# Kernel optimization log

Measured on AMD Instinct MI355X. Metric: run time of the kernel, lower is better.

Reference implementation:

```python
import jax, jax.numpy as jnp
import numpy as np

B, S, IN, OUT, H, M = 16, 512, 512, 512, 8, 4
HF = OUT // H  # head_feats = 64


def setup_inputs() -> dict:
    key = jax.random.key(0)
    ks = jax.random.split(key, 12)
    std = 0.02
    queries = jax.random.normal(ks[0], (B, S, IN), jnp.float32)
    keys = jax.random.normal(ks[1], (B, S, IN), jnp.float32)
    timespans = jax.random.uniform(ks[2], (B, S), jnp.float32)
    # causal mask tiled over heads*batch, matching [H*B, S, S] score shape
    attention_masks = jnp.broadcast_to(jnp.tril(jnp.ones((S, S), jnp.float32)), (H * B, S, S))
    event_marks = jax.random.uniform(ks[3], (H * B, 1, S, M), jnp.float32)
    Wq = std * jax.random.normal(ks[4], (IN, OUT), jnp.float32)
    Wk = std * jax.random.normal(ks[5], (IN, OUT), jnp.float32)
    Wv = std * jax.random.normal(ks[6], (IN, OUT), jnp.float32)
    Wt = std * jax.random.normal(ks[7], (IN, OUT), jnp.float32)
    Wi = std * jax.random.normal(ks[8], (HF + 1, M * HF), jnp.float32)  # fc_i weight
    bi = jnp.zeros((M * HF,), jnp.float32)                               # fc_i bias
    weight_i = std * jax.random.normal(ks[9], (M, HF), jnp.float32)
    scale_i = jnp.zeros((M,), jnp.float32)
    return {"queries": queries, "keys": keys, "timespans": timespans,
            "attention_masks": attention_masks, "event_marks": event_marks,
            "Wq": Wq, "Wk": Wk, "Wv": Wv, "Wt": Wt, "Wi": Wi, "bi": bi,
            "weight_i": weight_i, "scale_i": scale_i}


def reference(queries, keys, timespans, attention_masks, event_marks,
              Wq, Wk, Wv, Wt, Wi, bi, weight_i, scale_i):
    # torch's cat(chunk(X, H, dim=2), dim=0) == [B,S,H,HF] -> [H,B,S,HF] -> flat h*B+b
    def split_heads(X):
        return X.reshape(B, S, H, HF).transpose(2, 0, 1, 3)  # [H,B,S,HF]

    Q = split_heads(queries @ Wq)
    K = split_heads(keys @ Wk)
    V = split_heads(keys @ Wv)
    T = split_heads(keys @ Wt)

    scores = jnp.einsum('hbqf,hbkf->hbqk', Q, K) / jnp.sqrt(jnp.float32(OUT))
    mask = attention_masks.reshape(H, B, S, S)
    scores = jnp.where(mask == 0.0, jnp.float32(-2 ** 32 + 1), scores)
    attn = jax.nn.softmax(scores, axis=-1)  # [H,B,Sq,Sk]

    E = jnp.einsum('hbqk,hbkf->hbqf', attn, T)  # events fed to intensity net

    # --- Hawkes intensities ---
    ts = jnp.broadcast_to(timespans[None, :, :, None], (H, B, S, 1))
    mu = jax.nn.sigmoid(jnp.concatenate([E, ts], axis=-1) @ Wi + bi)  # [H,B,S,M*HF]
    mu = mu.reshape(H, B, S, M, HF)  # chunk over marks along feature dim
    scale = jnp.exp(scale_i)  # [M]
    lam = jnp.einsum('hbsmf,mf->hbsm', mu, weight_i) / scale
    lam = scale * jnp.log1p(jnp.exp(lam))  # scaled softplus, [H,B,S,M]

    # mark_inty[h,b,q,k] = sum_m lam[h,b,q,m] * event_marks[h,b,k,m]
    em = event_marks.reshape(H, B, S, M)
    mark_inty = jnp.einsum('hbqm,hbkm->hbqk', lam, em)

    out = jnp.einsum('hbqk,hbkf->hbqf', attn * mark_inty, V)
    out = out.transpose(1, 2, 0, 3).reshape(B, S, OUT) + queries[..., :OUT]
    all_mark_inty = lam.reshape(H * B, S, M)
    return out, all_mark_inty
```

## Files before the change

### kernel.cpp

```cpp
#include <hip/hip_runtime.h>
#include <math.h>

typedef __attribute__((ext_vector_type(8))) short short8;
typedef __attribute__((ext_vector_type(4))) float f32x4;

static __device__ __forceinline__ unsigned short f2bf(float f) {
  unsigned int u = __float_as_uint(f);
  u += 0x7FFFu + ((u >> 16) & 1u);
  return (unsigned short)(u >> 16);
}

static __device__ __forceinline__ void cp16(void* lds, const void* g) {
  __builtin_amdgcn_global_load_lds((const __attribute__((address_space(1))) void*)g,
                                   (__attribute__((address_space(3))) void*)lds,
                                   16, 0, 0);
}

__global__ __launch_bounds__(256) void convert_k(
    const float* __restrict__ Wq, const float* __restrict__ Wk,
    const float* __restrict__ Wv, const float* __restrict__ Wt,
    const float* __restrict__ Wi,
    unsigned short* __restrict__ Wb, unsigned short* __restrict__ WiF)
{
  __shared__ unsigned short tr[64 * 68];
  const int blk = blockIdx.x, tid = threadIdx.x;
  if (blk < 256) {
    int which = blk >> 6, tile = blk & 63;
    int r0 = (tile >> 3) << 6, c0 = (tile & 7) << 6;
    const float* W = (which == 0) ? Wq : (which == 1) ? Wk : (which == 2) ? Wv : Wt;
    const int rr = tid >> 4, cc = (tid & 15) << 2;
#pragma unroll
    for (int u = 0; u < 4; ++u) {
      int r = rr + u * 16;
      float4 v = *(const float4*)(W + (size_t)(r0 + r) * 512 + c0 + cc);
      tr[(cc + 0) * 68 + r] = f2bf(v.x);
      tr[(cc + 1) * 68 + r] = f2bf(v.y);
      tr[(cc + 2) * 68 + r] = f2bf(v.z);
      tr[(cc + 3) * 68 + r] = f2bf(v.w);
    }
    __syncthreads();
    unsigned short* dst = Wb + which * 262144;
#pragma unroll
    for (int u = 0; u < 4; ++u) {
      int c = rr + u * 16;
      ushort4 o = *(const ushort4*)&tr[c * 68 + cc];
      *(ushort4*)(dst + (size_t)(c0 + c) * 512 + r0 + cc) = o;
    }
  } else {
    int e = (blk - 256) * 256 + tid;
    int j = e & 7, ll = (e >> 3) & 63, r = e >> 9;
    int kk = r % 3, nt = r / 3;
    int col = nt * 16 + (ll & 15);
    int k = kk * 32 + (ll >> 4) * 8 + j;
    float val = (k < 64) ? Wi[k * 256 + col] : ((k == 64) ? Wi[16384 + col] : 0.0f);
    WiF[e] = f2bf(val);
  }
}

__global__ __launch_bounds__(256) void proj_mfma(
    const float* __restrict__ qin, const float* __restrict__ kin,
    const unsigned short* __restrict__ Wb,
    unsigned short* __restrict__ Qg, unsigned short* __restrict__ Kg,
    unsigned short* __restrict__ Vt, unsigned short* __restrict__ Tt)
{
  const int which = blockIdx.z;
  const float* A = (which == 0) ? qin : kin;
  const unsigned short* W = Wb + which * 262144;
  const int row0 = blockIdx.x * 128;
  const int col0 = blockIdx.y * 128;
  const int tid = threadIdx.x;
  const int wv = tid >> 6, l = tid & 63;
  const int quad = l >> 4, lc = l & 15;
  const int wm = wv >> 1, wn = wv & 1;

  __shared__ unsigned short Asm[2][128 * 32];
  __shared__ unsigned short Bsm[2][128 * 32];

  const int e2 = tid + 256;
  const int br0 = tid >> 2, bg0 = (tid & 3) ^ (br0 & 3);
  const int br1 = e2 >> 2,  bg1 = (e2 & 3) ^ (br1 & 3);
  f32x4 acc[4][4] = {};

  cp16(&Bsm[0][tid * 8], W + (size_t)(col0 + br0) * 512 + bg0 * 8);
  cp16(&Bsm[0][e2 * 8], W + (size_t)(col0 + br1) * 512 + bg1 * 8);
#pragma unroll
  for (int u = 0; u < 4; ++u) {
    int i = tid + u * 256, r = i >> 3, c4 = i & 7;
    float4 v = *(const float4*)(A + (size_t)(row0 + r) * 512 + c4 * 4);
    ushort4 o;
    o.x = f2bf(v.x); o.y = f2bf(v.y); o.z = f2bf(v.z); o.w = f2bf(v.w);
    *(ushort4*)&Asm[0][r * 32 + (((c4 >> 1) ^ (r & 3)) << 3) + ((c4 & 1) << 2)] = o;
  }
  __syncthreads();

  const int xk = lc & 3;
  for (int ks = 0; ks < 16; ++ks) {
    const int cur = ks & 1, nxt = cur ^ 1;
    float4 av[4];
    if (ks < 15) {
      const int k1 = (ks + 1) << 5;
      cp16(&Bsm[nxt][tid * 8], W + (size_t)(col0 + br0) * 512 + k1 + bg0 * 8);
      cp16(&Bsm[nxt][e2 * 8], W + (size_t)(col0 + br1) * 512 + k1 + bg1 * 8);
#pragma unroll
      for (int u = 0; u < 4; ++u) {
        int i = tid + u * 256, r = i >> 3, c4 = i & 7;
        av[u] = *(const float4*)(A + (size_t)(row0 + r) * 512 + k1 + c4 * 4);
      }
    }
    short8 a[4], b[4];
#pragma unroll
    for (int mi = 0; mi < 4; ++mi)
      a[mi] = *(const short8*)&Asm[cur][(wm * 64 + mi * 16 + lc) * 32 + ((quad ^ xk) << 3)];
#pragma unroll
    for (int nj = 0; nj < 4; ++nj)
      b[nj] = *(const short8*)&Bsm[cur][(wn * 64 + nj * 16 + lc) * 32 + ((quad ^ xk) << 3)];
#pragma unroll
    for (int mi = 0; mi < 4; ++mi)
#pragma unroll
      for (int nj = 0; nj < 4; ++nj)
        acc[mi][nj] = __builtin_amdgcn_mfma_f32_16x16x32_bf16(a[mi], b[nj], acc[mi][nj], 0, 0, 0);
    if (ks < 15) {
#pragma unroll
      for (int u = 0; u < 4; ++u) {
        int i = tid + u * 256, r = i >> 3, c4 = i & 7;
        ushort4 o;
        o.x = f2bf(av[u].x); o.y = f2bf(av[u].y); o.z = f2bf(av[u].z); o.w = f2bf(av[u].w);
        *(ushort4*)&Asm[nxt][r * 32 + (((c4 >> 1) ^ (r & 3)) << 3) + ((c4 & 1) << 2)] = o;
      }
    }
    __syncthreads();
  }

  const int h = (col0 >> 6) + wn;
  const int bidx = row0 >> 9;
  const int hb = h * 16 + bidx;
  if (which < 2) {
    unsigned short* C = (which == 0) ? Qg : Kg;
    const float os = (which == 0) ? 0.044194173824159216f : 1.0f;
#pragma unroll
    for (int mi = 0; mi < 4; ++mi) {
      int sbase = (row0 & 511) + wm * 64 + mi * 16 + quad * 4;
#pragma unroll
      for (int nj = 0; nj < 4; ++nj) {
        size_t base = (size_t)hb * 32768 + (size_t)sbase * 64 + nj * 16 + lc;
#pragma unroll
        for (int reg = 0; reg < 4; ++reg)
          C[base + (size_t)reg * 64] = f2bf(acc[mi][nj][reg] * os);
      }
    }
  } else {
    unsigned short* C = (which == 2) ? Vt : Tt;
    unsigned short* scr = wn ? Bsm[0] : Asm[0];
    const int sb = (row0 & 511) + wm * 64;
    __syncthreads();
#pragma unroll
    for (int round = 0; round < 2; ++round) {
      if (wm == round) {
#pragma unroll
        for (int mi = 0; mi < 4; ++mi)
#pragma unroll
          for (int nj = 0; nj < 4; ++nj)
#pragma unroll
            for (int reg = 0; reg < 4; ++reg) {
              int f = nj * 16 + lc, s = mi * 16 + quad * 4 + reg;
              int g = (s >> 3) ^ (f & 7);
              scr[f * 64 + g * 8 + (s & 7)] = f2bf(acc[mi][nj][reg]);
            }
#pragma unroll
        for (int it = 0; it < 8; ++it) {
          int fl = it * 8 + (l >> 3);
          int gg = (l & 7) ^ (fl & 7);
          short8 v = *(const short8*)&scr[fl * 64 + gg * 8];
          *(short8*)(C + (size_t)hb * 32768 + (size_t)fl * 512 + sb + (l & 7) * 8) = v;
        }
      }
      __syncthreads();
    }
  }
}

__global__ __launch_bounds__(256, 2) void attn_fused(
    const unsigned short* __restrict__ Qg, const unsigned short* __restrict__ Kg,
    const unsigned short* __restrict__ Vtg, const unsigned short* __restrict__ Ttg,
    const unsigned short* __restrict__ WiF,
    const float* __restrict__ bi, const float* __restrict__ wim,
    const float* __restrict__ sci, const float* __restrict__ tsp,
    const float* __restrict__ em, const float* __restrict__ queries,
    float* __restrict__ out, float* __restrict__ lamout)
{
  const int hb = blockIdx.x;
  const int y = blockIdx.y;
  const int qb = (y == 0) ? 3 : (y == 1) ? 2 : (y == 2) ? 0 : 1;
  const int q0 = qb << 7;
  const int kts = 2 * qb + 2;
  const int tid = threadIdx.x, wv = tid >> 6, l = tid & 63;
  const int quad = l >> 4, lc = l & 15;
  const int xg = lc & 7;

  __shared__ unsigned short Qs[8192];
  __shared__ unsigned short Ks[2][4096];
  __shared__ unsigned short TVs[2][4096];
  __shared__ unsigned short Wl[4][3072];
  __shared__ float emS[2][256];

  const int e1 = tid + 256;
  const int sr0 = tid >> 3, sg0 = (tid & 7) ^ (sr0 & 7);
  const int sr1 = e1 >> 3,  sg1 = (e1 & 7) ^ (sr1 & 7);
  const int sqk0 = sr0 * 64 + sg0 * 8,  sqk1 = sr1 * 64 + sg1 * 8;
  const int stv0 = sr0 * 512 + sg0 * 8, stv1 = sr1 * 512 + sg1 * 8;

  const unsigned short* KgB = Kg + (size_t)hb * 32768;
  const unsigned short* TgB = Ttg + (size_t)hb * 32768;
  const unsigned short* VgB = Vtg + (size_t)hb * 32768;

  const unsigned short* Qbase = Qg + (size_t)hb * 32768 + q0 * 64;
#pragma unroll
  for (int u = 0; u < 4; ++u) {
    int e = tid + u * 256;
    int r = e >> 3, g = (e & 7) ^ (r & 7);
    cp16(&Qs[e * 8], Qbase + r * 64 + g * 8);
  }
  cp16(&Ks[0][tid * 8], KgB + sqk0);
  cp16(&Ks[0][e1 * 8], KgB + sqk1);
  cp16(&TVs[0][tid * 8], TgB + stv0);
  cp16(&TVs[0][e1 * 8], TgB + stv1);
  __syncthreads();

  short8 aq[2][2];
#pragma unroll
  for (int rt = 0; rt < 2; ++rt)
#pragma unroll
    for (int kk = 0; kk < 2; ++kk)
      aq[rt][kk] = *(const short8*)&Qs[(wv * 32 + rt * 16 + lc) * 64 + ((kk * 4 + quad) ^ xg) * 8];

  f32x4 Eacc[2][4] = {};
  float lsum[2][4] = {};
  unsigned int Pc[8][16];

#pragma unroll
  for (int kt = 0; kt < 8; ++kt) {
    if (kt >= kts) continue;
    const int cur = kt & 1, nxt = cur ^ 1;
    const int k0 = kt << 6;
    if (kt + 1 < kts) {
      const int k1 = (kt + 1) << 6;
      cp16(&Ks[nxt][tid * 8], KgB + k1 * 64 + sqk0);
      cp16(&Ks[nxt][e1 * 8], KgB + k1 * 64 + sqk1);
      cp16(&TVs[nxt][tid * 8], TgB + k1 + stv0);
      cp16(&TVs[nxt][e1 * 8], TgB + k1 + stv1);
    }
    f32x4 sc[2][4] = {};
#pragma unroll
    for (int kk = 0; kk < 2; ++kk)
#pragma unroll
      for (int nj = 0; nj < 4; ++nj) {
        short8 b = *(const short8*)&Ks[cur][(nj * 16 + lc) * 64 + ((kk * 4 + quad) ^ xg) * 8];
        sc[0][nj] = __builtin_amdgcn_mfma_f32_16x16x32_bf16(aq[0][kk], b, sc[0][nj], 0, 0, 0);
        sc[1][nj] = __builtin_amdgcn_mfma_f32_16x16x32_bf16(aq[1][kk], b, sc[1][nj], 0, 0, 0);
      }
#pragma unroll
    for (int rt = 0; rt < 2; ++rt) {
      const int gq = q0 + wv * 32 + rt * 16 + quad * 4;
#pragma unroll
      for (int nj = 0; nj < 4; ++nj) {
        int col = nj * 16 + lc;
        unsigned short pb[4];
#pragma unroll
        for (int reg = 0; reg < 4; ++reg) {
          float pv = __expf(sc[rt][nj][reg]);
          if (k0 + col > gq + reg) pv = 0.0f;
          lsum[rt][reg] += pv;
          pb[reg] = f2bf(pv);
          int row = rt * 16 + quad * 4 + reg;
          int gp = (nj * 2 + (lc >> 3)) ^ (row & 7);
          Wl[wv][row * 96 + gp * 8 + (lc & 7)] = pb[reg];
        }
        Pc[kt][(rt * 4 + nj) * 2 + 0] = (unsigned int)pb[0] | ((unsigned int)pb[1] << 16);
        Pc[kt][(rt * 4 + nj) * 2 + 1] = (unsigned int)pb[2] | ((unsigned int)pb[3] << 16);
      }
    }
#pragma unroll
    for (int rt = 0; rt < 2; ++rt)
#pragma unroll
      for (int kk = 0; kk < 2; ++kk) {
        short8 a = *(const short8*)&Wl[wv][(rt * 16 + lc) * 96 + ((kk * 4 + quad) ^ xg) * 8];
#pragma unroll
        for (int fj = 0; fj < 4; ++fj) {
          short8 b = *(const short8*)&TVs[cur][(fj * 16 + lc) * 64 + ((kk * 4 + quad) ^ xg) * 8];
          Eacc[rt][fj] = __builtin_amdgcn_mfma_f32_16x16x32_bf16(a, b, Eacc[rt][fj], 0, 0, 0);
        }
      }
    __syncthreads();
  }

  float inv[2][4];
#pragma unroll
  for (int rt = 0; rt < 2; ++rt)
#pragma unroll
    for (int reg = 0; reg < 4; ++reg) {
      float s = lsum[rt][reg];
#pragma unroll
      for (int off = 1; off < 16; off <<= 1) s += __shfl_xor(s, off);
      inv[rt][reg] = 1.0f / s;
    }

  cp16(&Ks[0][tid * 8], VgB + stv0);
  cp16(&Ks[0][e1 * 8], VgB + stv1);
  emS[0][tid] = em[(size_t)hb * 2048 + tid];

#pragma unroll
  for (int rt = 0; rt < 2; ++rt)
#pragma unroll
    for (int reg = 0; reg < 4; ++reg) {
      int row = rt * 16 + quad * 4 + reg;
      int gq = q0 + wv * 32 + rt * 16 + quad * 4;
      unsigned short* rp = &Wl[wv][row * 96];
#pragma unroll
      for (int fj = 0; fj < 4; ++fj) {
        int gp = (fj * 2 + (lc >> 3)) ^ (row & 7);
        rp[gp * 8 + (lc & 7)] = f2bf(Eacc[rt][fj][reg] * inv[rt][reg]);
      }
      float tsv = (lc == 0) ? tsp[(hb & 15) * 512 + gq + reg] : 0.0f;
      int gt = 8 + ((lc >> 3) ^ (row & 3));
      rp[gt * 8 + (lc & 7)] = f2bf(tsv);
      int gz = 8 + ((2 + (lc >> 3)) ^ (row & 3));
      rp[gz * 8 + (lc & 7)] = 0;
    }

  float lam4[2][4][4];
#pragma unroll
  for (int rt = 0; rt < 2; ++rt) {
    short8 ia[3];
    ia[0] = *(const short8*)&Wl[wv][(rt * 16 + lc) * 96 + ((0 + quad) ^ xg) * 8];
    ia[1] = *(const short8*)&Wl[wv][(rt * 16 + lc) * 96 + ((4 + quad) ^ xg) * 8];
    ia[2] = *(const short8*)&Wl[wv][(rt * 16 + lc) * 96 + (8 + (quad ^ (lc & 3))) * 8];
    float lac[4][4] = {};
#pragma unroll
    for (int nt = 0; nt < 16; ++nt) {
      f32x4 iacc = {};
#pragma unroll
      for (int kk = 0; kk < 3; ++kk) {
        short8 b = *(const short8*)(WiF + ((nt * 3 + kk) * 64 + l) * 8);
        iacc = __builtin_amdgcn_mfma_f32_16x16x32_bf16(ia[kk], b, iacc, 0, 0, 0);
      }
      float bvv = bi[nt * 16 + lc];
      float wmv = wim[nt * 16 + lc];
#pragma unroll
      for (int reg = 0; reg < 4; ++reg) {
        float mu = 1.0f / (1.0f + __expf(-(iacc[reg] + bvv)));
        lac[reg][nt >> 2] += mu * wmv;
      }
    }
#pragma unroll
    for (int m = 0; m < 4; ++m) {
      float scv = __expf(sci[m]);
#pragma unroll
      for (int reg = 0; reg < 4; ++reg) {
        float s = lac[reg][m];
#pragma unroll
        for (int off = 1; off < 16; off <<= 1) s += __shfl_xor(s, off);
        float z = s / scv;
        float sp = (z > 20.0f) ? z : log1pf(__expf(z));
        lam4[rt][reg][m] = scv * sp;
      }
    }
    if (lc < 4) {
      int gq = q0 + wv * 32 + rt * 16 + quad * 4;
#pragma unroll
      for (int reg = 0; reg < 4; ++reg) {
        float v = (lc == 0) ? lam4[rt][reg][0] : (lc == 1) ? lam4[rt][reg][1]
                : (lc == 2) ? lam4[rt][reg][2] : lam4[rt][reg][3];
        lamout[((size_t)hb * 512 + gq + reg) * 4 + lc] = v;
      }
    }
#pragma unroll
    for (int reg = 0; reg < 4; ++reg)
#pragma unroll
      for (int m = 0; m < 4; ++m)
        lam4[rt][reg][m] *= inv[rt][reg];
  }
  __syncthreads();

  f32x4 Oacc[2][4] = {};
#pragma unroll
  for (int kt = 0; kt < 8; ++kt) {
    if (kt >= kts) continue;
    const int cur = kt & 1, nxt = cur ^ 1;
    if (kt + 1 < kts) {
      const int k1 = (kt + 1) << 6;
      cp16(&Ks[nxt][tid * 8], VgB + k1 + stv0);
      cp16(&Ks[nxt][e1 * 8], VgB + k1 + stv1);
      emS[nxt][tid] = em[(size_t)hb * 2048 + k1 * 4 + tid];
    }
#pragma unroll
    for (int rt = 0; rt < 2; ++rt) {
#pragma unroll
      for (int nj = 0; nj < 4; ++nj) {
        int col = nj * 16 + lc;
        float4 emv = *(const float4*)&emS[cur][col * 4];
        unsigned int u0 = Pc[kt][(rt * 4 + nj) * 2 + 0];
        unsigned int u1 = Pc[kt][(rt * 4 + nj) * 2 + 1];
        float p[4];
        p[0] = __uint_as_float(u0 << 16);
        p[1] = __uint_as_float(u0 & 0xFFFF0000u);
        p[2] = __uint_as_float(u1 << 16);
        p[3] = __uint_as_float(u1 & 0xFFFF0000u);
#pragma unroll
        for (int reg = 0; reg < 4; ++reg) {
          float mk = lam4[rt][reg][0] * emv.x + lam4[rt][reg][1] * emv.y +
                     lam4[rt][reg][2] * emv.z + lam4[rt][reg][3] * emv.w;
          int row = rt * 16 + quad * 4 + reg;
          int gp = (nj * 2 + (lc >> 3)) ^ (row & 7);
          Wl[wv][row * 96 + gp * 8 + (lc & 7)] = f2bf(p[reg] * mk);
        }
      }
    }
#pragma unroll
    for (int rt = 0; rt < 2; ++rt)
#pragma unroll
      for (int kk = 0; kk < 2; ++kk) {
        short8 a = *(const short8*)&Wl[wv][(rt * 16 + lc) * 96 + ((kk * 4 + quad) ^ xg) * 8];
#pragma unroll
        for (int fj = 0; fj < 4; ++fj) {
          short8 b = *(const short8*)&Ks[cur][(fj * 16 + lc) * 64 + ((kk * 4 + quad) ^ xg) * 8];
          Oacc[rt][fj] = __builtin_amdgcn_mfma_f32_16x16x32_bf16(a, b, Oacc[rt][fj], 0, 0, 0);
        }
      }
    __syncthreads();
  }

  const int h = hb >> 4, bidx = hb & 15;
#pragma unroll
  for (int rt = 0; rt < 2; ++rt) {
    const int gq = q0 + wv * 32 + rt * 16 + quad * 4;
#pragma unroll
    for (int reg = 0; reg < 4; ++reg) {
      size_t o = (size_t)bidx * 262144 + (size_t)(gq + reg) * 512 + h * 64 + lc;
#pragma unroll
      for (int fj = 0; fj < 4; ++fj)
        out[o + fj * 16] = Oacc[rt][fj][reg] + queries[o + fj * 16];
    }
  }
}

extern "C" void kernel_launch(void* const* d_in, const int* in_sizes, int n_in,
                              void* d_out, int out_size, void* d_ws, size_t ws_size,
                              hipStream_t stream)
{
  (void)in_sizes; (void)n_in; (void)out_size; (void)ws_size;
  const float* queries = (const float*)d_in[0];
  const float* keys    = (const float*)d_in[1];
  const float* tsp     = (const float*)d_in[2];
  const float* em      = (const float*)d_in[4];
  const float* Wq      = (const float*)d_in[5];
  const float* Wk      = (const float*)d_in[6];
  const float* Wv      = (const float*)d_in[7];
  const float* Wt      = (const float*)d_in[8];
  const float* Wi      = (const float*)d_in[9];
  const float* bi      = (const float*)d_in[10];
  const float* wim     = (const float*)d_in[11];
  const float* sci     = (const float*)d_in[12];
  float* out = (float*)d_out;

  char* w = (char*)d_ws;
  unsigned short* Qg  = (unsigned short*)(w + 0);
  unsigned short* Kg  = (unsigned short*)(w + 8388608);
  unsigned short* Vt  = (unsigned short*)(w + 16777216);
  unsigned short* Tt  = (unsigned short*)(w + 25165824);
  unsigned short* Wb  = (unsigned short*)(w + 33554432);
  unsigned short* WiF = (unsigned short*)(w + 35651584);

  convert_k<<<352, 256, 0, stream>>>(Wq, Wk, Wv, Wt, Wi, Wb, WiF);
  proj_mfma<<<dim3(64, 4, 4), 256, 0, stream>>>(queries, keys, Wb, Qg, Kg, Vt, Tt);
  attn_fused<<<dim3(128, 4), 256, 0, stream>>>(Qg, Kg, Vt, Tt, WiF, bi, wim, sci,
                                               tsp, em, queries, out,
                                               out + 4194304);
}
```

Before: 322.9 us.

## Recompute attention probabilities in second pass instead of caching in registers

The first pass no longer keeps the bf16 probabilities for every key tile in a large register array. The second pass reloads K tiles alongside V, redoes the QK^T MFMAs and the exp/mask, then applies the mark intensity. The aim is to cut register pressure and the fully unrolled 8-iteration loops so occupancy improves. The cost is doubled score MFMA and exp work plus extra K loads in the second pass.

```diff
diff --git a/kernel.cpp b/kernel.cpp
--- a/kernel.cpp
+++ b/kernel.cpp
@@ -235,11 +235,8 @@
 
   f32x4 Eacc[2][4] = {};
   float lsum[2][4] = {};
-  unsigned int Pc[8][16];
-
-#pragma unroll
-  for (int kt = 0; kt < 8; ++kt) {
-    if (kt >= kts) continue;
+
+  for (int kt = 0; kt < kts; ++kt) {
     const int cur = kt & 1, nxt = cur ^ 1;
     const int k0 = kt << 6;
     if (kt + 1 < kts) {
@@ -264,19 +261,15 @@
 #pragma unroll
       for (int nj = 0; nj < 4; ++nj) {
         int col = nj * 16 + lc;
-        unsigned short pb[4];
 #pragma unroll
         for (int reg = 0; reg < 4; ++reg) {
           float pv = __expf(sc[rt][nj][reg]);
           if (k0 + col > gq + reg) pv = 0.0f;
           lsum[rt][reg] += pv;
-          pb[reg] = f2bf(pv);
           int row = rt * 16 + quad * 4 + reg;
           int gp = (nj * 2 + (lc >> 3)) ^ (row & 7);
-          Wl[wv][row * 96 + gp * 8 + (lc & 7)] = pb[reg];
+          Wl[wv][row * 96 + gp * 8 + (lc & 7)] = f2bf(pv);
         }
-        Pc[kt][(rt * 4 + nj) * 2 + 0] = (unsigned int)pb[0] | ((unsigned int)pb[1] << 16);
-        Pc[kt][(rt * 4 + nj) * 2 + 1] = (unsigned int)pb[2] | ((unsigned int)pb[3] << 16);
       }
     }
 #pragma unroll
@@ -303,10 +296,6 @@
       for (int off = 1; off < 16; off <<= 1) s += __shfl_xor(s, off);
       inv[rt][reg] = 1.0f / s;
     }
-
-  cp16(&Ks[0][tid * 8], VgB + stv0);
-  cp16(&Ks[0][e1 * 8], VgB + stv1);
-  emS[0][tid] = em[(size_t)hb * 2048 + tid];
 
 #pragma unroll
   for (int rt = 0; rt < 2; ++rt)
@@ -379,39 +368,51 @@
       for (int m = 0; m < 4; ++m)
         lam4[rt][reg][m] *= inv[rt][reg];
   }
+
+  cp16(&Ks[0][tid * 8], KgB + sqk0);
+  cp16(&Ks[0][e1 * 8], KgB + sqk1);
+  cp16(&TVs[0][tid * 8], VgB + stv0);
+  cp16(&TVs[0][e1 * 8], VgB + stv1);
+  emS[0][tid] = em[(size_t)hb * 2048 + tid];
   __syncthreads();
 
   f32x4 Oacc[2][4] = {};
-#pragma unroll
-  for (int kt = 0; kt < 8; ++kt) {
-    if (kt >= kts) continue;
+  for (int kt = 0; kt < kts; ++kt) {
     const int cur = kt & 1, nxt = cur ^ 1;
+    const int k0 = kt << 6;
     if (kt + 1 < kts) {
       const int k1 = (kt + 1) << 6;
-      cp16(&Ks[nxt][tid * 8], VgB + k1 + stv0);
-      cp16(&Ks[nxt][e1 * 8], VgB + k1 + stv1);
+      cp16(&Ks[nxt][tid * 8], KgB + k1 * 64 + sqk0);
+      cp16(&Ks[nxt][e1 * 8], KgB + k1 * 64 + sqk1);
+      cp16(&TVs[nxt][tid * 8], VgB + k1 + stv0);
+      cp16(&TVs[nxt][e1 * 8], VgB + k1 + stv1);
       emS[nxt][tid] = em[(size_t)hb * 2048 + k1 * 4 + tid];
     }
+    f32x4 sc[2][4] = {};
+#pragma unroll
+    for (int kk = 0; kk < 2; ++kk)
+#pragma unroll
+      for (int nj = 0; nj < 4; ++nj) {
+        short8 b = *(const short8*)&Ks[cur][(nj * 16 + lc) * 64 + ((kk * 4 + quad) ^ xg) * 8];
+        sc[0][nj] = __builtin_amdgcn_mfma_f32_16x16x32_bf16(aq[0][kk], b, sc[0][nj], 0, 0, 0);
+        sc[1][nj] = __builtin_amdgcn_mfma_f32_16x16x32_bf16(aq[1][kk], b, sc[1][nj], 0, 0, 0);
+      }
 #pragma unroll
     for (int rt = 0; rt < 2; ++rt) {
+      const int gq = q0 + wv * 32 + rt * 16 + quad * 4;
 #pragma unroll
       for (int nj = 0; nj < 4; ++nj) {
         int col = nj * 16 + lc;
         float4 emv = *(const float4*)&emS[cur][col * 4];
-        unsigned int u0 = Pc[kt][(rt * 4 + nj) * 2 + 0];
-        unsigned int u1 = Pc[kt][(rt * 4 + nj) * 2 + 1];
-        float p[4];
-        p[0] = __uint_as_float(u0 << 16);
-        p[1] = __uint_as_float(u0 & 0xFFFF0000u);
-        p[2] = __uint_as_float(u1 << 16);
-        p[3] = __uint_as_float(u1 & 0xFFFF0000u);
 #pragma unroll
         for (int reg = 0; reg < 4; ++reg) {
+          float pv = __expf(sc[rt][nj][reg]);
+          if (k0 + col > gq + reg) pv = 0.0f;
           float mk = lam4[rt][reg][0] * emv.x + lam4[rt][reg][1] * emv.y +
                      lam4[rt][reg][2] * emv.z + lam4[rt][reg][3] * emv.w;
           int row = rt * 16 + quad * 4 + reg;
           int gp = (nj * 2 + (lc >> 3)) ^ (row & 7);
-          Wl[wv][row * 96 + gp * 8 + (lc & 7)] = f2bf(p[reg] * mk);
+          Wl[wv][row * 96 + gp * 8 + (lc & 7)] = f2bf(pv * mk);
         }
       }
     }
@@ -422,7 +423,7 @@
         short8 a = *(const short8*)&Wl[wv][(rt * 16 + lc) * 96 + ((kk * 4 + quad) ^ xg) * 8];
 #pragma unroll
         for (int fj = 0; fj < 4; ++fj) {
-          short8 b = *(const short8*)&Ks[cur][(fj * 16 + lc) * 64 + ((kk * 4 + quad) ^ xg) * 8];
+          short8 b = *(const short8*)&TVs[cur][(fj * 16 + lc) * 64 + ((kk * 4 + quad) ^ xg) * 8];
           Oacc[rt][fj] = __builtin_amdgcn_mfma_f32_16x16x32_bf16(a, b, Oacc[rt][fj], 0, 0, 0);
         }
       }
```

Result: faster. 307.0 us (-4.9%).
